# Kernel optimization log

Measured on AMD Instinct MI355X. Metric: run time of the kernel, lower is better.

The kernel has to match this reference:

```python
import jax, jax.numpy as jnp
import numpy as np

RATIO = 0.1

def setup_inputs() -> dict:
    key = jax.random.key(0)
    x = jax.random.normal(key, (8, 1024, 4096), dtype=jnp.float32)
    return {"x": x}

def reference(x):
    shape = x.shape
    xf = x.reshape(-1)                       # [N]
    k = int(RATIO * xf.shape[0])             # static k
    src, index = jax.lax.top_k(xf, k)         # values (not abs), matching torch.topk
    out = jnp.zeros_like(xf).at[index].set(src)
    return out.reshape(shape)
```

## Files before the change

### kernel.cpp

```cpp
#include <hip/hip_runtime.h>
#include <stdint.h>


#define EQ_CAP 65536

#define SC_WLO   0
#define SC_ABOVE 1
#define SC_TU    2
#define SC_NEED  3
#define SC_EQN   4
#define SC_OK    5
#define SC_FBHI  6
#define SC_FBKR  7
#define SC_SB    8
#define SC_SKR   9

__device__ __forceinline__ unsigned int f2u(float x) {
    unsigned int b = __float_as_uint(x);
    return (b & 0x80000000u) ? ~b : (b | 0x80000000u);
}
__device__ __forceinline__ float u2f(unsigned int u) {
    return __uint_as_float((u & 0x80000000u) ? (u & 0x7FFFFFFFu) : ~u);
}

__device__ __forceinline__ unsigned int block_exscan256(unsigned int v,
                                                        unsigned int* lds,
                                                        int tid)
{
    lds[tid] = v;
    __syncthreads();
    for (int off = 1; off < 256; off <<= 1) {
        unsigned int t = (tid >= off) ? lds[tid - off] : 0u;
        __syncthreads();
        lds[tid] += t;
        __syncthreads();
    }
    return lds[tid] - v;
}

__global__ void __launch_bounds__(256)
sample_kernel(const float* __restrict__ x, long long N,
              unsigned int* __restrict__ samp,
              unsigned int* __restrict__ histA)
{
    __shared__ unsigned int lh[2048];
    int tid = threadIdx.x;
    for (int i = tid; i < 2048; i += 256) lh[i] = 0u;
    __syncthreads();
    long long cstride = N / 256;
    long long idx = (long long)blockIdx.x * cstride + tid;
    if (idx >= N) idx = N - 1;
    unsigned int u = f2u(x[idx]);
    samp[blockIdx.x * 256 + tid] = u;
    atomicAdd(&lh[u >> 21], 1u);
    __syncthreads();
    for (int i = tid; i < 2048; i += 256) {
        unsigned int c = lh[i];
        if (c) atomicAdd(&histA[i], c);
    }
}

__global__ void __launch_bounds__(256)
scanA_kernel(const unsigned int* __restrict__ histA,
             unsigned int* __restrict__ sc, unsigned int ks)
{
    __shared__ unsigned int lds[256];
    int tid = threadIdx.x;
    unsigned int loc[8]; unsigned int part = 0u;
    for (int j = 0; j < 8; ++j) {
        unsigned int v = histA[2047 - (tid * 8 + j)];
        loc[j] = v; part += v;
    }
    unsigned int cum = block_exscan256(part, lds, tid);
    for (int j = 0; j < 8; ++j) {
        int bin = 2047 - (tid * 8 + j);
        unsigned int c = loc[j];
        if (cum < ks && cum + c >= ks) { sc[SC_SB] = (unsigned int)bin; sc[SC_SKR] = ks - cum; }
        cum += c;
    }
}

__global__ void __launch_bounds__(256)
sampleB_kernel(const unsigned int* __restrict__ samp,
               unsigned int* __restrict__ sc, unsigned int wbits)
{
    __shared__ unsigned int lh[2048];
    __shared__ unsigned int lds[256];
    int tid = threadIdx.x;
    for (int i = tid; i < 2048; i += 256) lh[i] = 0u;
    __syncthreads();
    unsigned int B = sc[SC_SB];
    unsigned int krem = sc[SC_SKR];
    for (int i = tid; i < 65536; i += 256) {
        unsigned int u = samp[i];
        if ((u >> 21) == B) atomicAdd(&lh[(u >> 10) & 2047u], 1u);
    }
    __syncthreads();
    unsigned int loc[8]; unsigned int part = 0u;
    for (int j = 0; j < 8; ++j) {
        unsigned int v = lh[2047 - (tid * 8 + j)];
        loc[j] = v; part += v;
    }
    unsigned int cum = block_exscan256(part, lds, tid);
    for (int j = 0; j < 8; ++j) {
        int bin = 2047 - (tid * 8 + j);
        unsigned int c = loc[j];
        if (cum < krem && cum + c >= krem) {
            unsigned int uhat = (B << 21) | ((unsigned int)bin << 10) | (1u << 9);
            unsigned int wsize = 1u << wbits;
            unsigned int half = wsize >> 1;
            unsigned int wlo = (uhat > half) ? (uhat - half) : 0u;
            unsigned int wlomax = (unsigned int)(0u - wsize);
            if (wlo > wlomax) wlo = wlomax;
            sc[SC_WLO] = wlo;
        }
        cum += c;
    }
}

__global__ void __launch_bounds__(256)
main_kernel(const float* __restrict__ x, int n4, long long N,
            unsigned int* __restrict__ fine,
            unsigned int* __restrict__ fbz,
            unsigned int* __restrict__ sc, unsigned int wbits)
{
    __shared__ unsigned int wsum[4];
    int tid = threadIdx.x;
    int g = blockIdx.x * blockDim.x + tid;
    if (g < 131072) fbz[g] = 0u;
    unsigned int wlo = sc[SC_WLO];
    unsigned int whiM1 = wlo + (1u << wbits) - 1u;
    const float4* x4 = (const float4*)x;
    int stride = gridDim.x * blockDim.x;
    unsigned int above = 0u;
    for (int i = g; i < n4; i += stride) {
        float4 v = x4[i];
        unsigned int u;
        u = f2u(v.x); if (u > whiM1) ++above; else if (u >= wlo) atomicAdd(&fine[u - wlo], 1u);
        u = f2u(v.y); if (u > whiM1) ++above; else if (u >= wlo) atomicAdd(&fine[u - wlo], 1u);
        u = f2u(v.z); if (u > whiM1) ++above; else if (u >= wlo) atomicAdd(&fine[u - wlo], 1u);
        u = f2u(v.w); if (u > whiM1) ++above; else if (u >= wlo) atomicAdd(&fine[u - wlo], 1u);
    }
    long long t0 = (long long)n4 * 4;
    if (blockIdx.x == 0 && tid < (int)(N - t0)) {
        unsigned int u = f2u(x[t0 + tid]);
        if (u > whiM1) ++above; else if (u >= wlo) atomicAdd(&fine[u - wlo], 1u);
    }
    for (int o = 32; o; o >>= 1) above += __shfl_down(above, o, 64);
    if ((tid & 63) == 0) wsum[tid >> 6] = above;
    __syncthreads();
    if (tid == 0) {
        unsigned int s = wsum[0] + wsum[1] + wsum[2] + wsum[3];
        if (s) atomicAdd(&sc[SC_ABOVE], s);
    }
}

__global__ void __launch_bounds__(256)
chunksum_kernel(const unsigned int* __restrict__ fine,
                unsigned int* __restrict__ chunk_sums)
{
    __shared__ unsigned int p[256];
    int tid = threadIdx.x;
    const unsigned int* base = fine + (size_t)blockIdx.x * 1024;
    unsigned int s = 0u;
    for (int i = tid; i < 1024; i += 256) s += base[i];
    p[tid] = s;
    __syncthreads();
    for (int o = 128; o; o >>= 1) { if (tid < o) p[tid] += p[tid + o]; __syncthreads(); }
    if (tid == 0) chunk_sums[blockIdx.x] = p[0];
}

__global__ void __launch_bounds__(256)
final_kernel(const unsigned int* __restrict__ fine,
             const unsigned int* __restrict__ chunk_sums,
             unsigned int* __restrict__ sc, unsigned int k, int nchunk)
{
    __shared__ unsigned int lds[256];
    __shared__ unsigned int sh[3];
    __shared__ unsigned int s_total;
    int tid = threadIdx.x;
    unsigned int above = sc[SC_ABOVE];
    int seg = nchunk >> 8;
    unsigned int part = 0u;
    for (int j = 0; j < seg; ++j) part += chunk_sums[nchunk - 1 - (tid * seg + j)];
    unsigned int ex = block_exscan256(part, lds, tid);
    if (tid == 255) s_total = ex + part;
    __syncthreads();
    unsigned int total = s_total;
    unsigned int valid = (above < k) && ((k - above) <= total);
    if (tid == 0) sc[SC_OK] = valid;
    if (!valid) return;
    unsigned int krem = k - above;
    unsigned int cum = ex;
    for (int j = 0; j < seg; ++j) {
        int c = nchunk - 1 - (tid * seg + j);
        unsigned int cc = chunk_sums[c];
        if (cum < krem && cum + cc >= krem) { sh[0] = (unsigned int)c; sh[1] = krem - cum; }
        cum += cc;
    }
    __syncthreads();
    unsigned int C = sh[0], krem2 = sh[1];
    unsigned int loc[4]; unsigned int p2 = 0u;
    for (int j = 0; j < 4; ++j) {
        unsigned int v = fine[(size_t)C * 1024 + (1023 - (tid * 4 + j))];
        loc[j] = v; p2 += v;
    }
    __syncthreads();
    unsigned int ex2 = block_exscan256(p2, lds, tid);
    unsigned int cum2 = ex2;
    for (int j = 0; j < 4; ++j) {
        int bin = 1023 - (tid * 4 + j);
        unsigned int cc = loc[j];
        if (cum2 < krem2 && cum2 + cc >= krem2) {
            sc[SC_TU] = sc[SC_WLO] + C * 1024u + (unsigned int)bin;
            sc[SC_NEED] = krem2 - cum2;
        }
        cum2 += cc;
    }
}

__global__ void __launch_bounds__(256)
fb_hist_kernel(const float* __restrict__ x, int n4, long long N,
               unsigned int* __restrict__ hist,
               const unsigned int* __restrict__ sc, int lowpass)
{
    if (sc[SC_OK]) return;
    unsigned int pref = lowpass ? sc[SC_FBHI] : 0u;
    const float4* x4 = (const float4*)x;
    int stride = gridDim.x * blockDim.x;
    for (int i = blockIdx.x * blockDim.x + threadIdx.x; i < n4; i += stride) {
        float4 v = x4[i];
        unsigned int u;
        #define FB_ONE(c) u = f2u(c); \
            if (!lowpass) atomicAdd(&hist[u >> 16], 1u); \
            else if ((u >> 16) == pref) atomicAdd(&hist[u & 0xFFFFu], 1u);
        FB_ONE(v.x) FB_ONE(v.y) FB_ONE(v.z) FB_ONE(v.w)
        #undef FB_ONE
    }
    long long t0 = (long long)n4 * 4;
    if (blockIdx.x == 0 && threadIdx.x < (int)(N - t0)) {
        unsigned int u = f2u(x[t0 + threadIdx.x]);
        if (!lowpass) atomicAdd(&hist[u >> 16], 1u);
        else if ((u >> 16) == pref) atomicAdd(&hist[u & 0xFFFFu], 1u);
    }
}

__global__ void __launch_bounds__(256)
fb_scan_kernel(const unsigned int* __restrict__ hist,
               unsigned int* __restrict__ sc, int lowpass, unsigned int k)
{
    if (sc[SC_OK]) return;
    __shared__ unsigned int lds[256];
    int tid = threadIdx.x;
    unsigned int krem = lowpass ? sc[SC_FBKR] : k;
    unsigned int part = 0u;
    for (int j = 0; j < 256; ++j) part += hist[65535 - (tid * 256 + j)];
    unsigned int ex = block_exscan256(part, lds, tid);
    unsigned int cum = ex;
    for (int j = 0; j < 256; ++j) {
        int bin = 65535 - (tid * 256 + j);
        unsigned int cc = hist[bin];
        if (cum < krem && cum + cc >= krem) {
            if (!lowpass) { sc[SC_FBHI] = (unsigned int)bin; sc[SC_FBKR] = krem - cum; }
            else { sc[SC_TU] = (sc[SC_FBHI] << 16) | (unsigned int)bin; sc[SC_NEED] = krem - cum; }
        }
        cum += cc;
    }
}

__global__ void __launch_bounds__(256)
scatter_kernel(const float* __restrict__ x, int n4, long long N,
               float* __restrict__ out, unsigned int* __restrict__ sc,
               unsigned int* __restrict__ eq_list, int cap)
{
    int tid = threadIdx.x;
    unsigned int tu = sc[SC_TU];
    const float4* x4 = (const float4*)x;
    float4* o4 = (float4*)out;
    int stride = gridDim.x * blockDim.x;
    for (int i = blockIdx.x * blockDim.x + tid; i < n4; i += stride) {
        float4 v = x4[i];
        unsigned int u0 = f2u(v.x), u1 = f2u(v.y), u2 = f2u(v.z), u3 = f2u(v.w);
        float4 o;
        o.x = (u0 > tu) ? v.x : 0.0f;
        o.y = (u1 > tu) ? v.y : 0.0f;
        o.z = (u2 > tu) ? v.z : 0.0f;
        o.w = (u3 > tu) ? v.w : 0.0f;
        if (u0 == tu || u1 == tu || u2 == tu || u3 == tu) {
            unsigned int b = (unsigned int)i * 4u;
            if (u0 == tu) { unsigned int p = atomicAdd(&sc[SC_EQN], 1u); if (p < (unsigned int)cap) eq_list[p] = b + 0u; }
            if (u1 == tu) { unsigned int p = atomicAdd(&sc[SC_EQN], 1u); if (p < (unsigned int)cap) eq_list[p] = b + 1u; }
            if (u2 == tu) { unsigned int p = atomicAdd(&sc[SC_EQN], 1u); if (p < (unsigned int)cap) eq_list[p] = b + 2u; }
            if (u3 == tu) { unsigned int p = atomicAdd(&sc[SC_EQN], 1u); if (p < (unsigned int)cap) eq_list[p] = b + 3u; }
        }
        o4[i] = o;
    }
    long long t0 = (long long)n4 * 4;
    if (blockIdx.x == 0 && tid < (int)(N - t0)) {
        long long idx = t0 + tid;
        float v = x[idx];
        unsigned int u = f2u(v);
        out[idx] = (u > tu) ? v : 0.0f;
        if (u == tu) { unsigned int p = atomicAdd(&sc[SC_EQN], 1u); if (p < (unsigned int)cap) eq_list[p] = (unsigned int)idx; }
    }
}

__global__ void __launch_bounds__(256)
eqfix_kernel(float* __restrict__ out, const unsigned int* __restrict__ sc,
             const unsigned int* __restrict__ eq_list, int cap)
{
    unsigned int m = sc[SC_EQN]; if (m > (unsigned int)cap) m = (unsigned int)cap;
    unsigned int need = sc[SC_NEED];
    unsigned int tu = sc[SC_TU];
    float f = u2f(tu);
    for (unsigned int j = threadIdx.x; j < m; j += blockDim.x) {
        unsigned int idx = eq_list[j];
        unsigned int cnt = 0u;
        for (unsigned int l = 0; l < m; ++l) cnt += (eq_list[l] < idx) ? 1u : 0u;
        if (cnt < need) out[idx] = f;
    }
}

extern "C" void kernel_launch(void* const* d_in, const int* in_sizes, int n_in,
                              void* d_out, int out_size, void* d_ws, size_t ws_size,
                              hipStream_t stream) {
    const float* x = (const float*)d_in[0];
    float* out = (float*)d_out;
    long long N = (long long)in_sizes[0];
    int n4 = (int)(N >> 2);
    unsigned int k = (unsigned int)((double)N * 0.1);
    if (k == 0u) k = 1u;

    unsigned int NS = 65536u;
    unsigned int ks = (unsigned int)((double)NS * (double)k / (double)N);
    if (ks < 1u) ks = 1u; if (ks > NS) ks = NS;

    unsigned int wbits = 20;
    if (ws_size < ((size_t)2u << 20) + ((size_t)4u << 20)) wbits = 18;
    int nchunk = 1 << (wbits - 10);

    uint8_t* w = (uint8_t*)d_ws;
    unsigned int* sc         = (unsigned int*)w;
    unsigned int* histA      = (unsigned int*)(w + 1024);
    unsigned int* chunk_sums = (unsigned int*)(w + 9216);
    unsigned int* samp       = (unsigned int*)(w + 32768);
    unsigned int* eq_list    = (unsigned int*)(w + 294912);
    unsigned int* fbz        = (unsigned int*)(w + 557056);
    unsigned int* fbA        = fbz;
    unsigned int* fbB        = fbz + 65536;
    unsigned int* fine       = (unsigned int*)(w + ((size_t)2u << 20));

    hipMemsetAsync(w, 0, 16384, stream);
    hipMemsetAsync(fine, 0, (size_t)4u << wbits, stream);

    sample_kernel<<<256, 256, 0, stream>>>(x, N, samp, histA);
    scanA_kernel<<<1, 256, 0, stream>>>(histA, sc, ks);
    sampleB_kernel<<<1, 256, 0, stream>>>(samp, sc, wbits);

    main_kernel<<<2048, 256, 0, stream>>>(x, n4, N, fine, fbz, sc, wbits);
    chunksum_kernel<<<nchunk, 256, 0, stream>>>(fine, chunk_sums);
    final_kernel<<<1, 256, 0, stream>>>(fine, chunk_sums, sc, k, nchunk);

    fb_hist_kernel<<<1024, 256, 0, stream>>>(x, n4, N, fbA, sc, 0);
    fb_scan_kernel<<<1, 256, 0, stream>>>(fbA, sc, 0, k);
    fb_hist_kernel<<<1024, 256, 0, stream>>>(x, n4, N, fbB, sc, 1);
    fb_scan_kernel<<<1, 256, 0, stream>>>(fbB, sc, 1, k);

    scatter_kernel<<<2048, 256, 0, stream>>>(x, n4, N, out, sc, eq_list, EQ_CAP);
    eqfix_kernel<<<1, 256, 0, stream>>>(out, sc, eq_list, EQ_CAP);
}
```

Before: 361.8 us.

## Fuse histogram and output write into one pass with candidate lists

The main pass now writes the output directly, zeroing all but clearly-above elements, and buffers near-threshold candidates in LDS before flushing them to per-segment global lists. A fix kernel then writes candidates above the threshold and collects ties from those lists, so the second full read of x in the scatter kernel is avoided on the common path. A coarse global histogram is built during the same pass so the fallback needs only one extra pass instead of two. Sampling and refinement kernels are merged, and the memsets are replaced by zeroing inside the prep kernel. The cost is extra LDS atomics per element and overflow checks, with a fallback path when the candidate capacity is exceeded.

```diff
diff --git a/kernel.cpp b/kernel.cpp
--- a/kernel.cpp
+++ b/kernel.cpp
@@ -2,7 +2,13 @@
 #include <stdint.h>
 
 
+#define WBITS 20u
+#define WSIZE (1u << WBITS)
+#define SEG 64
+#define SEGCAP 32768
 #define EQ_CAP 65536
+#define MAIN_GRID 2048
+#define BLK 256
 
 #define SC_WLO   0
 #define SC_ABOVE 1
@@ -10,10 +16,9 @@
 #define SC_NEED  3
 #define SC_EQN   4
 #define SC_OK    5
-#define SC_FBHI  6
-#define SC_FBKR  7
-#define SC_SB    8
-#define SC_SKR   9
+#define SC_CB    6
+#define SC_CBKR  7
+#define SC_OVF   8
 
 __device__ __forceinline__ unsigned int f2u(float x) {
     unsigned int b = __float_as_uint(x);
@@ -39,78 +44,61 @@
 }
 
 __global__ void __launch_bounds__(256)
-sample_kernel(const float* __restrict__ x, long long N,
-              unsigned int* __restrict__ samp,
-              unsigned int* __restrict__ histA)
+prep_kernel(const float* __restrict__ x, long long N,
+            unsigned int* __restrict__ samp,
+            unsigned int* __restrict__ fine,
+            unsigned int* __restrict__ hist2,
+            unsigned int* __restrict__ small)
+{
+    int g = blockIdx.x * 256 + threadIdx.x;
+    if (g < 8192) small[g] = 0u;
+    for (int i = g; i < (1 << 20); i += 65536) fine[i] = 0u;
+    for (int i = g; i < (1 << 21); i += 65536) hist2[i] = 0u;
+    long long cstride = N >> 8; if (cstride < 1) cstride = 1;
+    long long idx = (long long)blockIdx.x * cstride + threadIdx.x;
+    if (idx >= N) idx = N - 1;
+    samp[g] = f2u(x[idx]);
+}
+
+__global__ void __launch_bounds__(256)
+refine_kernel(const unsigned int* __restrict__ samp,
+              unsigned int* __restrict__ sc, unsigned int ks, unsigned int NS)
 {
     __shared__ unsigned int lh[2048];
+    __shared__ unsigned int lds[256];
+    __shared__ unsigned int sB, sKr;
     int tid = threadIdx.x;
     for (int i = tid; i < 2048; i += 256) lh[i] = 0u;
     __syncthreads();
-    long long cstride = N / 256;
-    long long idx = (long long)blockIdx.x * cstride + tid;
-    if (idx >= N) idx = N - 1;
-    unsigned int u = f2u(x[idx]);
-    samp[blockIdx.x * 256 + tid] = u;
-    atomicAdd(&lh[u >> 21], 1u);
-    __syncthreads();
-    for (int i = tid; i < 2048; i += 256) {
-        unsigned int c = lh[i];
-        if (c) atomicAdd(&histA[i], c);
-    }
-}
-
-__global__ void __launch_bounds__(256)
-scanA_kernel(const unsigned int* __restrict__ histA,
-             unsigned int* __restrict__ sc, unsigned int ks)
-{
-    __shared__ unsigned int lds[256];
-    int tid = threadIdx.x;
-    unsigned int loc[8]; unsigned int part = 0u;
-    for (int j = 0; j < 8; ++j) {
-        unsigned int v = histA[2047 - (tid * 8 + j)];
-        loc[j] = v; part += v;
-    }
+    for (unsigned int i = tid; i < NS; i += 256) atomicAdd(&lh[samp[i] >> 21], 1u);
+    __syncthreads();
+    unsigned int loc[8], part = 0u;
+    for (int j = 0; j < 8; ++j) { unsigned int v = lh[2047 - (tid * 8 + j)]; loc[j] = v; part += v; }
     unsigned int cum = block_exscan256(part, lds, tid);
     for (int j = 0; j < 8; ++j) {
-        int bin = 2047 - (tid * 8 + j);
-        unsigned int c = loc[j];
-        if (cum < ks && cum + c >= ks) { sc[SC_SB] = (unsigned int)bin; sc[SC_SKR] = ks - cum; }
+        int bin = 2047 - (tid * 8 + j); unsigned int c = loc[j];
+        if (cum < ks && cum + c >= ks) { sB = (unsigned int)bin; sKr = ks - cum; }
         cum += c;
     }
-}
-
-__global__ void __launch_bounds__(256)
-sampleB_kernel(const unsigned int* __restrict__ samp,
-               unsigned int* __restrict__ sc, unsigned int wbits)
-{
-    __shared__ unsigned int lh[2048];
-    __shared__ unsigned int lds[256];
-    int tid = threadIdx.x;
+    __syncthreads();
+    unsigned int B = sB, kr = sKr;
     for (int i = tid; i < 2048; i += 256) lh[i] = 0u;
     __syncthreads();
-    unsigned int B = sc[SC_SB];
-    unsigned int krem = sc[SC_SKR];
-    for (int i = tid; i < 65536; i += 256) {
+    for (unsigned int i = tid; i < NS; i += 256) {
         unsigned int u = samp[i];
         if ((u >> 21) == B) atomicAdd(&lh[(u >> 10) & 2047u], 1u);
     }
     __syncthreads();
-    unsigned int loc[8]; unsigned int part = 0u;
+    part = 0u;
+    for (int j = 0; j < 8; ++j) { unsigned int v = lh[2047 - (tid * 8 + j)]; loc[j] = v; part += v; }
+    cum = block_exscan256(part, lds, tid);
     for (int j = 0; j < 8; ++j) {
-        unsigned int v = lh[2047 - (tid * 8 + j)];
-        loc[j] = v; part += v;
-    }
-    unsigned int cum = block_exscan256(part, lds, tid);
-    for (int j = 0; j < 8; ++j) {
-        int bin = 2047 - (tid * 8 + j);
-        unsigned int c = loc[j];
-        if (cum < krem && cum + c >= krem) {
-            unsigned int uhat = (B << 21) | ((unsigned int)bin << 10) | (1u << 9);
-            unsigned int wsize = 1u << wbits;
-            unsigned int half = wsize >> 1;
+        int bin = 2047 - (tid * 8 + j); unsigned int c = loc[j];
+        if (cum < kr && cum + c >= kr) {
+            unsigned int uhat = (B << 21) | ((unsigned int)bin << 10) | 512u;
+            unsigned int half = WSIZE >> 1;
             unsigned int wlo = (uhat > half) ? (uhat - half) : 0u;
-            unsigned int wlomax = (unsigned int)(0u - wsize);
+            unsigned int wlomax = 0u - WSIZE;
             if (wlo > wlomax) wlo = wlomax;
             sc[SC_WLO] = wlo;
         }
@@ -119,32 +107,50 @@
 }
 
 __global__ void __launch_bounds__(256)
-main_kernel(const float* __restrict__ x, int n4, long long N,
-            unsigned int* __restrict__ fine,
-            unsigned int* __restrict__ fbz,
-            unsigned int* __restrict__ sc, unsigned int wbits)
-{
+main_kernel(const float* __restrict__ x, float* __restrict__ out,
+            int n4, long long N,
+            unsigned int* __restrict__ fine, unsigned int* __restrict__ csum,
+            unsigned int* __restrict__ gcoarse,
+            unsigned int* __restrict__ segctr, uint2* __restrict__ list,
+            unsigned int* __restrict__ sc)
+{
+    __shared__ unsigned int coarse[2048];
+    __shared__ unsigned int bidx[2048];
+    __shared__ unsigned int bval[2048];
+    __shared__ unsigned int bcnt, bbase, bovf;
     __shared__ unsigned int wsum[4];
     int tid = threadIdx.x;
-    int g = blockIdx.x * blockDim.x + tid;
-    if (g < 131072) fbz[g] = 0u;
-    unsigned int wlo = sc[SC_WLO];
-    unsigned int whiM1 = wlo + (1u << wbits) - 1u;
+    for (int i = tid; i < 2048; i += 256) coarse[i] = 0u;
+    if (tid == 0) { bcnt = 0u; bovf = 0u; }
+    __syncthreads();
+    unsigned int wlo = sc[SC_WLO], whi = wlo + WSIZE - 1u;
     const float4* x4 = (const float4*)x;
+    float4* o4 = (float4*)out;
     int stride = gridDim.x * blockDim.x;
     unsigned int above = 0u;
-    for (int i = g; i < n4; i += stride) {
-        float4 v = x4[i];
-        unsigned int u;
-        u = f2u(v.x); if (u > whiM1) ++above; else if (u >= wlo) atomicAdd(&fine[u - wlo], 1u);
-        u = f2u(v.y); if (u > whiM1) ++above; else if (u >= wlo) atomicAdd(&fine[u - wlo], 1u);
-        u = f2u(v.z); if (u > whiM1) ++above; else if (u >= wlo) atomicAdd(&fine[u - wlo], 1u);
-        u = f2u(v.w); if (u > whiM1) ++above; else if (u >= wlo) atomicAdd(&fine[u - wlo], 1u);
+    for (int i = blockIdx.x * blockDim.x + tid; i < n4; i += stride) {
+        float4 v = x4[i]; float4 o; unsigned int b = (unsigned int)i * 4u;
+        #define DO(comp, oc, lane) { unsigned int u = f2u(comp); \
+            atomicAdd(&coarse[u >> 21], 1u); \
+            if (u > whi) { oc = comp; ++above; } \
+            else { oc = 0.0f; if (u >= wlo) { \
+                unsigned int p = atomicAdd(&bcnt, 1u); \
+                if (p < 2048u) { bidx[p] = b + lane; bval[p] = u; } else bovf = 1u; } } }
+        DO(v.x, o.x, 0u) DO(v.y, o.y, 1u) DO(v.z, o.z, 2u) DO(v.w, o.w, 3u)
+        #undef DO
+        o4[i] = o;
     }
     long long t0 = (long long)n4 * 4;
     if (blockIdx.x == 0 && tid < (int)(N - t0)) {
-        unsigned int u = f2u(x[t0 + tid]);
-        if (u > whiM1) ++above; else if (u >= wlo) atomicAdd(&fine[u - wlo], 1u);
+        long long idx = t0 + tid; float v = x[idx]; unsigned int u = f2u(v);
+        atomicAdd(&coarse[u >> 21], 1u);
+        float o = 0.0f;
+        if (u > whi) { o = v; ++above; }
+        else if (u >= wlo) {
+            unsigned int p = atomicAdd(&bcnt, 1u);
+            if (p < 2048u) { bidx[p] = (unsigned int)idx; bval[p] = u; } else bovf = 1u;
+        }
+        out[idx] = o;
     }
     for (int o = 32; o; o >>= 1) above += __shfl_down(above, o, 64);
     if ((tid & 63) == 0) wsum[tid >> 6] = above;
@@ -152,127 +158,178 @@
     if (tid == 0) {
         unsigned int s = wsum[0] + wsum[1] + wsum[2] + wsum[3];
         if (s) atomicAdd(&sc[SC_ABOVE], s);
-    }
-}
-
-__global__ void __launch_bounds__(256)
-chunksum_kernel(const unsigned int* __restrict__ fine,
-                unsigned int* __restrict__ chunk_sums)
-{
-    __shared__ unsigned int p[256];
-    int tid = threadIdx.x;
-    const unsigned int* base = fine + (size_t)blockIdx.x * 1024;
-    unsigned int s = 0u;
-    for (int i = tid; i < 1024; i += 256) s += base[i];
-    p[tid] = s;
-    __syncthreads();
-    for (int o = 128; o; o >>= 1) { if (tid < o) p[tid] += p[tid + o]; __syncthreads(); }
-    if (tid == 0) chunk_sums[blockIdx.x] = p[0];
+        unsigned int cnt = bcnt > 2048u ? 2048u : bcnt;
+        unsigned int base = 0u;
+        if (cnt) base = atomicAdd(&segctr[(blockIdx.x & 63u) * 16u], cnt);
+        bbase = base;
+        if (bovf || bcnt > 2048u || base + cnt > (unsigned int)SEGCAP)
+            atomicAdd(&sc[SC_OVF], 1u);
+    }
+    __syncthreads();
+    unsigned int cnt = bcnt > 2048u ? 2048u : bcnt;
+    unsigned int base = bbase;
+    uint2* mylist = list + (size_t)(blockIdx.x & 63u) * SEGCAP;
+    for (unsigned int j = tid; j < cnt; j += 256u) {
+        unsigned int pos = base + j;
+        if (pos < (unsigned int)SEGCAP) mylist[pos] = make_uint2(bidx[j], bval[j]);
+        unsigned int off = bval[j] - wlo;
+        atomicAdd(&fine[off], 1u);
+        atomicAdd(&csum[off >> 10], 1u);
+    }
+    for (int i = tid; i < 2048; i += 256) {
+        unsigned int c = coarse[i];
+        if (c) atomicAdd(&gcoarse[i], c);
+    }
 }
 
 __global__ void __launch_bounds__(256)
 final_kernel(const unsigned int* __restrict__ fine,
-             const unsigned int* __restrict__ chunk_sums,
-             unsigned int* __restrict__ sc, unsigned int k, int nchunk)
+             const unsigned int* __restrict__ csum,
+             const unsigned int* __restrict__ gcoarse,
+             unsigned int* __restrict__ sc, unsigned int k)
 {
     __shared__ unsigned int lds[256];
-    __shared__ unsigned int sh[3];
+    __shared__ unsigned int sh2[2];
     __shared__ unsigned int s_total;
     int tid = threadIdx.x;
     unsigned int above = sc[SC_ABOVE];
-    int seg = nchunk >> 8;
-    unsigned int part = 0u;
-    for (int j = 0; j < seg; ++j) part += chunk_sums[nchunk - 1 - (tid * seg + j)];
+    unsigned int ovf = sc[SC_OVF];
+    unsigned int loc[4], part = 0u;
+    for (int j = 0; j < 4; ++j) { unsigned int v = csum[1023 - (tid * 4 + j)]; loc[j] = v; part += v; }
     unsigned int ex = block_exscan256(part, lds, tid);
     if (tid == 255) s_total = ex + part;
     __syncthreads();
-    unsigned int total = s_total;
-    unsigned int valid = (above < k) && ((k - above) <= total);
+    unsigned int wtot = s_total;
+    unsigned int valid = (!ovf) && (above < k) && ((k - above) <= wtot);
     if (tid == 0) sc[SC_OK] = valid;
+    {
+        unsigned int l2[8], p2 = 0u;
+        for (int j = 0; j < 8; ++j) { unsigned int v = gcoarse[2047 - (tid * 8 + j)]; l2[j] = v; p2 += v; }
+        __syncthreads();
+        unsigned int e2 = block_exscan256(p2, lds, tid);
+        unsigned int cum = e2;
+        for (int j = 0; j < 8; ++j) {
+            int bin = 2047 - (tid * 8 + j); unsigned int c = l2[j];
+            if (cum < k && cum + c >= k) { sc[SC_CB] = (unsigned int)bin; sc[SC_CBKR] = k - cum; }
+            cum += c;
+        }
+    }
     if (!valid) return;
     unsigned int krem = k - above;
+    __syncthreads();
     unsigned int cum = ex;
-    for (int j = 0; j < seg; ++j) {
-        int c = nchunk - 1 - (tid * seg + j);
-        unsigned int cc = chunk_sums[c];
-        if (cum < krem && cum + cc >= krem) { sh[0] = (unsigned int)c; sh[1] = krem - cum; }
+    for (int j = 0; j < 4; ++j) {
+        int c = 1023 - (tid * 4 + j); unsigned int cc = loc[j];
+        if (cum < krem && cum + cc >= krem) { sh2[0] = (unsigned int)c; sh2[1] = krem - cum; }
         cum += cc;
     }
     __syncthreads();
-    unsigned int C = sh[0], krem2 = sh[1];
-    unsigned int loc[4]; unsigned int p2 = 0u;
+    unsigned int C = sh2[0], kr2 = sh2[1];
+    unsigned int l3[4], p3 = 0u;
+    for (int j = 0; j < 4; ++j) { unsigned int v = fine[C * 1024u + (1023u - (tid * 4 + j))]; l3[j] = v; p3 += v; }
+    __syncthreads();
+    unsigned int e3 = block_exscan256(p3, lds, tid);
+    unsigned int cum3 = e3;
     for (int j = 0; j < 4; ++j) {
-        unsigned int v = fine[(size_t)C * 1024 + (1023 - (tid * 4 + j))];
-        loc[j] = v; p2 += v;
-    }
-    __syncthreads();
-    unsigned int ex2 = block_exscan256(p2, lds, tid);
-    unsigned int cum2 = ex2;
-    for (int j = 0; j < 4; ++j) {
-        int bin = 1023 - (tid * 4 + j);
-        unsigned int cc = loc[j];
-        if (cum2 < krem2 && cum2 + cc >= krem2) {
-            sc[SC_TU] = sc[SC_WLO] + C * 1024u + (unsigned int)bin;
-            sc[SC_NEED] = krem2 - cum2;
-        }
-        cum2 += cc;
-    }
-}
-
-__global__ void __launch_bounds__(256)
-fb_hist_kernel(const float* __restrict__ x, int n4, long long N,
-               unsigned int* __restrict__ hist,
-               const unsigned int* __restrict__ sc, int lowpass)
+        unsigned int bin = 1023u - (tid * 4 + j); unsigned int cc = l3[j];
+        if (cum3 < kr2 && cum3 + cc >= kr2) { sc[SC_TU] = sc[SC_WLO] + C * 1024u + bin; sc[SC_NEED] = kr2 - cum3; }
+        cum3 += cc;
+    }
+}
+
+__global__ void __launch_bounds__(256)
+fix_kernel(const float* __restrict__ x, float* __restrict__ out,
+           int n4, long long N,
+           const unsigned int* __restrict__ segctr, const uint2* __restrict__ list,
+           unsigned int* __restrict__ hist2, unsigned int* __restrict__ csum2,
+           unsigned int* __restrict__ eq_list, unsigned int* __restrict__ sc)
+{
+    int tid = threadIdx.x;
+    if (sc[SC_OK]) {
+        unsigned int tu = sc[SC_TU];
+        unsigned int seg = blockIdx.x & 63u, sub = blockIdx.x >> 6;
+        unsigned int cnt = segctr[seg * 16u]; if (cnt > (unsigned int)SEGCAP) cnt = SEGCAP;
+        const uint2* mylist = list + (size_t)seg * SEGCAP;
+        for (unsigned int j = sub * 256u + tid; j < cnt; j += 32u * 256u) {
+            uint2 e = mylist[j];
+            if (e.y > tu) out[e.x] = u2f(e.y);
+            else if (e.y == tu) {
+                unsigned int p = atomicAdd(&sc[SC_EQN], 1u);
+                if (p < (unsigned int)EQ_CAP) eq_list[p] = e.x;
+            }
+        }
+    } else {
+        unsigned int CB = sc[SC_CB];
+        const float4* x4 = (const float4*)x;
+        int stride = gridDim.x * blockDim.x;
+        for (int i = blockIdx.x * blockDim.x + tid; i < n4; i += stride) {
+            float4 v = x4[i];
+            #define FB(c) { unsigned int u = f2u(c); if ((u >> 21) == CB) { \
+                unsigned int off = u & 0x1FFFFFu; atomicAdd(&hist2[off], 1u); atomicAdd(&csum2[off >> 10], 1u); } }
+            FB(v.x) FB(v.y) FB(v.z) FB(v.w)
+            #undef FB
+        }
+        long long t0 = (long long)n4 * 4;
+        if (blockIdx.x == 0 && tid < (int)(N - t0)) {
+            unsigned int u = f2u(x[t0 + tid]);
+            if ((u >> 21) == CB) {
+                unsigned int off = u & 0x1FFFFFu;
+                atomicAdd(&hist2[off], 1u); atomicAdd(&csum2[off >> 10], 1u);
+            }
+        }
+    }
+}
+
+__global__ void __launch_bounds__(256)
+post_kernel(const unsigned int* __restrict__ hist2,
+            const unsigned int* __restrict__ csum2,
+            float* __restrict__ out, const unsigned int* __restrict__ eq_list,
+            unsigned int* __restrict__ sc)
+{
+    __shared__ unsigned int lds[256];
+    __shared__ unsigned int sh2[2];
+    int tid = threadIdx.x;
+    if (sc[SC_OK]) {
+        unsigned int m = sc[SC_EQN]; if (m > (unsigned int)EQ_CAP) m = EQ_CAP;
+        unsigned int need = sc[SC_NEED];
+        float f = u2f(sc[SC_TU]);
+        for (unsigned int j = tid; j < m; j += 256u) {
+            unsigned int idx = eq_list[j]; unsigned int c = 0u;
+            for (unsigned int l = 0; l < m; ++l) c += (eq_list[l] < idx) ? 1u : 0u;
+            if (c < need) out[idx] = f;
+        }
+    } else {
+        unsigned int CB = sc[SC_CB], kr = sc[SC_CBKR];
+        unsigned int loc[8], part = 0u;
+        for (int j = 0; j < 8; ++j) { unsigned int v = csum2[2047 - (tid * 8 + j)]; loc[j] = v; part += v; }
+        unsigned int ex = block_exscan256(part, lds, tid);
+        unsigned int cum = ex;
+        for (int j = 0; j < 8; ++j) {
+            int c = 2047 - (tid * 8 + j); unsigned int cc = loc[j];
+            if (cum < kr && cum + cc >= kr) { sh2[0] = (unsigned int)c; sh2[1] = kr - cum; }
+            cum += cc;
+        }
+        __syncthreads();
+        unsigned int C2 = sh2[0], kr2 = sh2[1];
+        unsigned int l3[4], p3 = 0u;
+        for (int j = 0; j < 4; ++j) { unsigned int v = hist2[C2 * 1024u + (1023u - (tid * 4 + j))]; l3[j] = v; p3 += v; }
+        __syncthreads();
+        unsigned int e3 = block_exscan256(p3, lds, tid);
+        unsigned int cum3 = e3;
+        for (int j = 0; j < 4; ++j) {
+            unsigned int bin = 1023u - (tid * 4 + j); unsigned int cc = l3[j];
+            if (cum3 < kr2 && cum3 + cc >= kr2) { sc[SC_TU] = (CB << 21) | (C2 * 1024u + bin); sc[SC_NEED] = kr2 - cum3; }
+            cum3 += cc;
+        }
+    }
+}
+
+__global__ void __launch_bounds__(256)
+fb_scatter_kernel(const float* __restrict__ x, int n4, long long N,
+                  float* __restrict__ out, unsigned int* __restrict__ sc,
+                  unsigned int* __restrict__ eq_list)
 {
     if (sc[SC_OK]) return;
-    unsigned int pref = lowpass ? sc[SC_FBHI] : 0u;
-    const float4* x4 = (const float4*)x;
-    int stride = gridDim.x * blockDim.x;
-    for (int i = blockIdx.x * blockDim.x + threadIdx.x; i < n4; i += stride) {
-        float4 v = x4[i];
-        unsigned int u;
-        #define FB_ONE(c) u = f2u(c); \
-            if (!lowpass) atomicAdd(&hist[u >> 16], 1u); \
-            else if ((u >> 16) == pref) atomicAdd(&hist[u & 0xFFFFu], 1u);
-        FB_ONE(v.x) FB_ONE(v.y) FB_ONE(v.z) FB_ONE(v.w)
-        #undef FB_ONE
-    }
-    long long t0 = (long long)n4 * 4;
-    if (blockIdx.x == 0 && threadIdx.x < (int)(N - t0)) {
-        unsigned int u = f2u(x[t0 + threadIdx.x]);
-        if (!lowpass) atomicAdd(&hist[u >> 16], 1u);
-        else if ((u >> 16) == pref) atomicAdd(&hist[u & 0xFFFFu], 1u);
-    }
-}
-
-__global__ void __launch_bounds__(256)
-fb_scan_kernel(const unsigned int* __restrict__ hist,
-               unsigned int* __restrict__ sc, int lowpass, unsigned int k)
-{
-    if (sc[SC_OK]) return;
-    __shared__ unsigned int lds[256];
-    int tid = threadIdx.x;
-    unsigned int krem = lowpass ? sc[SC_FBKR] : k;
-    unsigned int part = 0u;
-    for (int j = 0; j < 256; ++j) part += hist[65535 - (tid * 256 + j)];
-    unsigned int ex = block_exscan256(part, lds, tid);
-    unsigned int cum = ex;
-    for (int j = 0; j < 256; ++j) {
-        int bin = 65535 - (tid * 256 + j);
-        unsigned int cc = hist[bin];
-        if (cum < krem && cum + cc >= krem) {
-            if (!lowpass) { sc[SC_FBHI] = (unsigned int)bin; sc[SC_FBKR] = krem - cum; }
-            else { sc[SC_TU] = (sc[SC_FBHI] << 16) | (unsigned int)bin; sc[SC_NEED] = krem - cum; }
-        }
-        cum += cc;
-    }
-}
-
-__global__ void __launch_bounds__(256)
-scatter_kernel(const float* __restrict__ x, int n4, long long N,
-               float* __restrict__ out, unsigned int* __restrict__ sc,
-               unsigned int* __restrict__ eq_list, int cap)
-{
     int tid = threadIdx.x;
     unsigned int tu = sc[SC_TU];
     const float4* x4 = (const float4*)x;
@@ -288,36 +345,34 @@
         o.w = (u3 > tu) ? v.w : 0.0f;
         if (u0 == tu || u1 == tu || u2 == tu || u3 == tu) {
             unsigned int b = (unsigned int)i * 4u;
-            if (u0 == tu) { unsigned int p = atomicAdd(&sc[SC_EQN], 1u); if (p < (unsigned int)cap) eq_list[p] = b + 0u; }
-            if (u1 == tu) { unsigned int p = atomicAdd(&sc[SC_EQN], 1u); if (p < (unsigned int)cap) eq_list[p] = b + 1u; }
-            if (u2 == tu) { unsigned int p = atomicAdd(&sc[SC_EQN], 1u); if (p < (unsigned int)cap) eq_list[p] = b + 2u; }
-            if (u3 == tu) { unsigned int p = atomicAdd(&sc[SC_EQN], 1u); if (p < (unsigned int)cap) eq_list[p] = b + 3u; }
+            if (u0 == tu) { unsigned int p = atomicAdd(&sc[SC_EQN], 1u); if (p < (unsigned int)EQ_CAP) eq_list[p] = b + 0u; }
+            if (u1 == tu) { unsigned int p = atomicAdd(&sc[SC_EQN], 1u); if (p < (unsigned int)EQ_CAP) eq_list[p] = b + 1u; }
+            if (u2 == tu) { unsigned int p = atomicAdd(&sc[SC_EQN], 1u); if (p < (unsigned int)EQ_CAP) eq_list[p] = b + 2u; }
+            if (u3 == tu) { unsigned int p = atomicAdd(&sc[SC_EQN], 1u); if (p < (unsigned int)EQ_CAP) eq_list[p] = b + 3u; }
         }
         o4[i] = o;
     }
     long long t0 = (long long)n4 * 4;
     if (blockIdx.x == 0 && tid < (int)(N - t0)) {
         long long idx = t0 + tid;
-        float v = x[idx];
-        unsigned int u = f2u(v);
+        float v = x[idx]; unsigned int u = f2u(v);
         out[idx] = (u > tu) ? v : 0.0f;
-        if (u == tu) { unsigned int p = atomicAdd(&sc[SC_EQN], 1u); if (p < (unsigned int)cap) eq_list[p] = (unsigned int)idx; }
-    }
-}
-
-__global__ void __launch_bounds__(256)
-eqfix_kernel(float* __restrict__ out, const unsigned int* __restrict__ sc,
-             const unsigned int* __restrict__ eq_list, int cap)
-{
-    unsigned int m = sc[SC_EQN]; if (m > (unsigned int)cap) m = (unsigned int)cap;
+        if (u == tu) { unsigned int p = atomicAdd(&sc[SC_EQN], 1u); if (p < (unsigned int)EQ_CAP) eq_list[p] = (unsigned int)idx; }
+    }
+}
+
+__global__ void __launch_bounds__(256)
+fb_post_kernel(float* __restrict__ out, const unsigned int* __restrict__ sc,
+               const unsigned int* __restrict__ eq_list)
+{
+    if (sc[SC_OK]) return;
+    unsigned int m = sc[SC_EQN]; if (m > (unsigned int)EQ_CAP) m = EQ_CAP;
     unsigned int need = sc[SC_NEED];
-    unsigned int tu = sc[SC_TU];
-    float f = u2f(tu);
+    float f = u2f(sc[SC_TU]);
     for (unsigned int j = threadIdx.x; j < m; j += blockDim.x) {
-        unsigned int idx = eq_list[j];
-        unsigned int cnt = 0u;
-        for (unsigned int l = 0; l < m; ++l) cnt += (eq_list[l] < idx) ? 1u : 0u;
-        if (cnt < need) out[idx] = f;
+        unsigned int idx = eq_list[j]; unsigned int c = 0u;
+        for (unsigned int l = 0; l < m; ++l) c += (eq_list[l] < idx) ? 1u : 0u;
+        if (c < need) out[idx] = f;
     }
 }
 
@@ -335,37 +390,26 @@
     unsigned int ks = (unsigned int)((double)NS * (double)k / (double)N);
     if (ks < 1u) ks = 1u; if (ks > NS) ks = NS;
 
-    unsigned int wbits = 20;
-    if (ws_size < ((size_t)2u << 20) + ((size_t)4u << 20)) wbits = 18;
-    int nchunk = 1 << (wbits - 10);
-
     uint8_t* w = (uint8_t*)d_ws;
-    unsigned int* sc         = (unsigned int*)w;
-    unsigned int* histA      = (unsigned int*)(w + 1024);
-    unsigned int* chunk_sums = (unsigned int*)(w + 9216);
-    unsigned int* samp       = (unsigned int*)(w + 32768);
-    unsigned int* eq_list    = (unsigned int*)(w + 294912);
-    unsigned int* fbz        = (unsigned int*)(w + 557056);
-    unsigned int* fbA        = fbz;
-    unsigned int* fbB        = fbz + 65536;
-    unsigned int* fine       = (unsigned int*)(w + ((size_t)2u << 20));
-
-    hipMemsetAsync(w, 0, 16384, stream);
-    hipMemsetAsync(fine, 0, (size_t)4u << wbits, stream);
-
-    sample_kernel<<<256, 256, 0, stream>>>(x, N, samp, histA);
-    scanA_kernel<<<1, 256, 0, stream>>>(histA, sc, ks);
-    sampleB_kernel<<<1, 256, 0, stream>>>(samp, sc, wbits);
-
-    main_kernel<<<2048, 256, 0, stream>>>(x, n4, N, fine, fbz, sc, wbits);
-    chunksum_kernel<<<nchunk, 256, 0, stream>>>(fine, chunk_sums);
-    final_kernel<<<1, 256, 0, stream>>>(fine, chunk_sums, sc, k, nchunk);
-
-    fb_hist_kernel<<<1024, 256, 0, stream>>>(x, n4, N, fbA, sc, 0);
-    fb_scan_kernel<<<1, 256, 0, stream>>>(fbA, sc, 0, k);
-    fb_hist_kernel<<<1024, 256, 0, stream>>>(x, n4, N, fbB, sc, 1);
-    fb_scan_kernel<<<1, 256, 0, stream>>>(fbB, sc, 1, k);
-
-    scatter_kernel<<<2048, 256, 0, stream>>>(x, n4, N, out, sc, eq_list, EQ_CAP);
-    eqfix_kernel<<<1, 256, 0, stream>>>(out, sc, eq_list, EQ_CAP);
-}
+    unsigned int* sc      = (unsigned int*)w;
+    unsigned int* segctr  = (unsigned int*)(w + 1024);
+    unsigned int* csum    = (unsigned int*)(w + 8192);
+    unsigned int* csum2   = (unsigned int*)(w + 16384);
+    unsigned int* gcoarse = (unsigned int*)(w + 24576);
+    unsigned int* eq_list = (unsigned int*)(w + 32768);
+    unsigned int* samp    = (unsigned int*)(w + 294912);
+    unsigned int* fine    = (unsigned int*)(w + ((size_t)1 << 20));
+    unsigned int* hist2   = (unsigned int*)(w + ((size_t)8 << 20));
+    uint2*        list    = (uint2*)       (w + ((size_t)16 << 20));
+
+    prep_kernel<<<256, BLK, 0, stream>>>(x, N, samp, fine, hist2, sc);
+    refine_kernel<<<1, BLK, 0, stream>>>(samp, sc, ks, NS);
+    main_kernel<<<MAIN_GRID, BLK, 0, stream>>>(x, out, n4, N, fine, csum,
+                                               gcoarse, segctr, list, sc);
+    final_kernel<<<1, BLK, 0, stream>>>(fine, csum, gcoarse, sc, k);
+    fix_kernel<<<MAIN_GRID, BLK, 0, stream>>>(x, out, n4, N, segctr, list,
+                                              hist2, csum2, eq_list, sc);
+    post_kernel<<<1, BLK, 0, stream>>>(hist2, csum2, out, eq_list, sc);
+    fb_scatter_kernel<<<MAIN_GRID, BLK, 0, stream>>>(x, n4, N, out, sc, eq_list);
+    fb_post_kernel<<<1, BLK, 0, stream>>>(out, sc, eq_list);
+}
```

New measurement: 544.5 us. 50.5% more time.
